# Performance work log

Measured on AMD Instinct MI355X. Metric: run time of the kernel, lower is better.

## Reference

```python
import jax, jax.numpy as jnp
import numpy as np

BLOCK_SIZE = 64
WINDOW_SIZE = 512
TOPK_BLOCKS = 16
NEG = -1e30


def setup_inputs() -> dict:
    key = jax.random.key(0)
    ks = jax.random.split(key, 6)
    B, T, D = 4, 8192, 256
    return {
        "queries": jax.random.normal(ks[0], (B, T, D), jnp.float32),
        "keys": jax.random.normal(ks[1], (B, T, D), jnp.float32),
        "values": jax.random.normal(ks[2], (B, T, D), jnp.float32),
        "gate_cmp": jax.random.uniform(ks[3], (B, T), jnp.float32),
        "gate_slc": jax.random.uniform(ks[4], (B, T), jnp.float32),
        "gate_swa": jax.random.uniform(ks[5], (B, T), jnp.float32),
    }


def _compress(x, bs):
    # mean-pool tokens into blocks of size bs (pad tail with zeros like F.pad)
    B, T, D = x.shape
    n_blocks = -(-T // bs)
    pad = n_blocks * bs - T
    if pad > 0:
        x = jnp.pad(x, ((0, 0), (0, pad), (0, 0)))
    return x.reshape(B, n_blocks, bs, D).mean(axis=2)  # [B, n_blocks, D]


def _selective(queries, comp_K, comp_V, gate):
    B, T, D = queries.shape
    nb = comp_K.shape[1]
    scale = D ** -0.5
    scores = jnp.einsum("btd,bnd->btn", queries, comp_K) * scale  # [B,T,nb]
    block_ids = jnp.arange(T) // BLOCK_SIZE                       # query's block
    allowed = jnp.arange(nb)[None, :] <= block_ids[:, None]       # no future blocks
    scores = jnp.where(allowed[None], scores, NEG)
    probs = jax.nn.softmax(scores, axis=-1)
    k = min(TOPK_BLOCKS, nb)
    topk_vals, topk_inds = jax.lax.top_k(probs, k)                # [B,T,k]
    gathered = jax.vmap(lambda cv, idx: cv[idx])(comp_V, topk_inds)  # [B,T,k,D]
    sel = jnp.einsum("btk,btkd->btd", topk_vals, gathered)
    return sel * gate[..., None]


def _sliding(queries, keys, values, gate):
    # block-banded sliding-window attention: each query attends to the last
    # WINDOW_SIZE tokens (inclusive of itself), computed per query-block of
    # size W over a 2W key window [block_start - W, block_end).
    B, T, D = queries.shape
    W = WINDOW_SIZE
    n = T // W
    scale = D ** -0.5
    k_pad = jnp.pad(keys, ((0, 0), (W, 0), (0, 0)))   # [B, T+W, D]
    v_pad = jnp.pad(values, ((0, 0), (W, 0), (0, 0)))
    idx = jnp.arange(n)[:, None] * W + jnp.arange(2 * W)[None, :]  # [n, 2W]
    k_win = k_pad[:, idx]                              # [B, n, 2W, D]
    v_win = v_pad[:, idx]
    q_blk = queries.reshape(B, n, W, D)
    scores = jnp.einsum("bnwd,bncd->bnwc", q_blk, k_win) * scale  # [B,n,W,2W]
    r = jnp.arange(W)[:, None]       # row within block
    c = jnp.arange(2 * W)[None, :]   # col within window
    base = (c <= r + W) & (c >= r + 1)                        # [W, 2W] band
    pos_ok = (jnp.arange(n)[:, None, None] * W + c[None] - W) >= 0  # [n,1,2W]
    mask = base[None] & pos_ok                                 # [n, W, 2W]
    scores = jnp.where(mask[None], scores, NEG)
    attn = jax.nn.softmax(scores, axis=-1)
    out = jnp.einsum("bnwc,bncd->bnwd", attn, v_win).reshape(B, T, D)
    return out * gate[..., None]


def reference(queries, keys, values, gate_cmp, gate_slc, gate_swa):
    D = queries.shape[-1]
    scale = D ** -0.5
    comp_K = _compress(keys, BLOCK_SIZE)
    comp_V = _compress(values, BLOCK_SIZE)
    # compressed branch (note: no causal mask, faithful to the source)
    raw = jnp.einsum("btd,bnd->btn", queries, comp_K) * scale
    comp_out = jnp.einsum("btn,bnd->btd", jax.nn.softmax(raw, axis=-1), comp_V)
    comp_out = comp_out * gate_cmp[..., None]
    sel_out = _selective(queries, comp_K, comp_V, gate_slc)
    slide_out = _sliding(queries, keys, values, gate_swa)
    return comp_out + sel_out + slide_out
```

## Files before the change

kernel.cpp:

```cpp
#include <hip/hip_runtime.h>
#include <hip/hip_bf16.h>

#define Tlen 8192
#define Dd 256
#define NBc 128

typedef __attribute__((ext_vector_type(4))) float f32x4;
typedef __attribute__((ext_vector_type(8))) short bf16x8;

__device__ __forceinline__ unsigned short f2bf(float f){
  unsigned u = __builtin_bit_cast(unsigned, f);
  u += 0x7fffu + ((u >> 16) & 1u);
  return (unsigned short)(u >> 16);
}
__device__ __forceinline__ f32x4 mfma16(bf16x8 a, bf16x8 b, f32x4 c){
  return __builtin_amdgcn_mfma_f32_16x16x32_bf16(a, b, c, 0, 0, 0);
}
__device__ __forceinline__ void bar(){
  asm volatile("" ::: "memory");
  __builtin_amdgcn_s_barrier();
  asm volatile("" ::: "memory");
}
__device__ __forceinline__ bf16x8 pack8(f32x4 a0, f32x4 a1){
  bf16x8 o;
  o[0]=(short)f2bf(a0[0]); o[1]=(short)f2bf(a0[1]); o[2]=(short)f2bf(a0[2]); o[3]=(short)f2bf(a0[3]);
  o[4]=(short)f2bf(a1[0]); o[5]=(short)f2bf(a1[1]); o[6]=(short)f2bf(a1[2]); o[7]=(short)f2bf(a1[3]);
  return o;
}
#define GLL16(g, l) __builtin_amdgcn_global_load_lds( \
    (const __attribute__((address_space(1))) unsigned int*)(const void*)(g), \
    (__attribute__((address_space(3))) unsigned int*)(void*)(l), 16, 0, 0)

template<int C>
__device__ __forceinline__ int dppi(int x){
  return __builtin_amdgcn_update_dpp(x, x, C, 0xF, 0xF, false);
}
template<int C>
__device__ __forceinline__ float dppf(float x){
  return __builtin_bit_cast(float, dppi<C>(__builtin_bit_cast(int, x)));
}
__device__ __forceinline__ float dpp_sum16(float x){
  x += dppf<0x121>(x); x += dppf<0x122>(x); x += dppf<0x124>(x); x += dppf<0x128>(x);
  return x;
}

__device__ __forceinline__ bf16x8 load_qfrag(const float* qrow, int kc, int g){
  f32x4 v0 = *(const f32x4*)(qrow + kc*32 + g*8);
  f32x4 v1 = *(const f32x4*)(qrow + kc*32 + g*8 + 4);
  return pack8(v0, v1);
}

__global__ __launch_bounds__(256) void k_prep(const float* __restrict__ K, const float* __restrict__ V,
    unsigned short* __restrict__ ck, unsigned short* __restrict__ cvt,
    unsigned short* __restrict__ Vswz, unsigned short* __restrict__ Kswz, int do_k){
  __shared__ unsigned short Lt[64][72];
  int b = blockIdx.x >> 7, blk = blockIdx.x & 127;
  int t = threadIdx.x;
  const float* Kb = K + ((size_t)b*Tlen + (size_t)blk*64)*Dd;
  const float* Vb = V + ((size_t)b*Tlen + (size_t)blk*64)*Dd;
  {
    float sk=0.f, sv=0.f;
    #pragma unroll 8
    for (int i=0;i<64;i++){ sk += Kb[(size_t)i*Dd + t]; sv += Vb[(size_t)i*Dd + t]; }
    ck[((size_t)b*NBc + blk)*Dd + (((t>>3) ^ (blk&7))<<3) + (t&7)] = f2bf(sk*(1.f/64.f));
    cvt[((size_t)b*Dd + t)*NBc + blk] = f2bf(sv*(1.f/64.f));
  }
  if (do_k){
    unsigned short* kd = Kswz + ((size_t)(b*NBc + blk))*16384;
    #pragma unroll
    for (int i=0;i<8;i++){
      int id = i*256 + t, r = id>>5, c = id&31;
      f32x4 a0 = *(const f32x4*)(Kb + (size_t)r*Dd + c*8);
      f32x4 a1 = *(const f32x4*)(Kb + (size_t)r*Dd + c*8 + 4);
      *(bf16x8*)(kd + r*256 + ((c ^ (r&7))*8)) = pack8(a0,a1);
    }
  }
  unsigned short* vd = Vswz + ((size_t)(b*NBc + blk))*16384;
  for (int dt=0; dt<4; ++dt){
    __syncthreads();
    #pragma unroll
    for (int it=0; it<4; ++it){
      int idx = it*256 + t, r = idx>>4, c4 = idx&15;
      f32x4 v = *(const f32x4*)(Vb + (size_t)r*Dd + dt*64 + c4*4);
      #pragma unroll
      for (int ii=0;ii<4;ii++) Lt[c4*4+ii][r] = f2bf(v[ii]);
    }
    __syncthreads();
    int dd = t>>2, ch = t&3, d = dt*64 + dd;
    unsigned short tmp[16];
    #pragma unroll
    for (int u=0;u<16;u++) tmp[u] = Lt[dd][ch*16+u];
    *(bf16x8*)(vd + d*64 + (((ch*2  ) ^ (d&7))*8)) = *(bf16x8*)(tmp);
    *(bf16x8*)(vd + d*64 + (((ch*2+1) ^ (d&7))*8)) = *(bf16x8*)(tmp+8);
  }
}

__device__ __forceinline__ void compsel_phase(unsigned short* LB,
    const float* Q, const unsigned short* ck, const unsigned short* cvt,
    const float* gc, const float* gs, float* out, int b, int tile, bool first){
  int q0 = tile*64;
  int t = threadIdx.x, w = t >> 6, l = t & 63, g = l >> 4, lr = l & 15;
  int tr = w >> 1, half = w & 1;

  float gcv[2], gsv[2];
  #pragma unroll
  for (int jl=0;jl<2;jl++){
    int qq = q0 + tr*16 + 4*g + half*2 + jl;
    gcv[jl] = gc[(size_t)b*Tlen + qq];
    gsv[jl] = gs[(size_t)b*Tlen + qq];
  }
  bf16x8 qa[8];
  const float* qrow = Q + ((size_t)b*Tlen + q0 + tr*16 + lr)*Dd;
  #pragma unroll
  for (int kc=0;kc<8;kc++) qa[kc] = load_qfrag(qrow, kc, g);

  __syncthreads();

  {
    const unsigned short* src = ck + (size_t)b*NBc*Dd;
    #pragma unroll
    for (int i=0;i<8;i++){
      int idx = i*512 + t;
      GLL16(src + idx*8, &LB[idx*8]);
    }
  }
  asm volatile("s_waitcnt vmcnt(0)" ::: "memory");
  bar();

  f32x4 acc[8];
  #pragma unroll
  for (int nf=0;nf<8;nf++) acc[nf] = f32x4{0.f,0.f,0.f,0.f};
  #pragma unroll
  for (int nf=0;nf<8;nf++){
    int row = nf*16+lr;
    const unsigned short* rbase = &LB[row*256];
    int xk = row & 7;
    #pragma unroll
    for (int kc=0;kc<8;kc++){
      bf16x8 bb = *(const bf16x8*)(rbase + (((kc*4+g) ^ xk)*8));
      acc[nf] = mfma16(qa[kc], bb, acc[nf]);
    }
  }
  #pragma unroll
  for (int nf=0;nf<8;nf++) acc[nf] *= 0.0625f;
  asm volatile("s_waitcnt lgkmcnt(0)" ::: "memory");
  bar();

  bool al[8];
  #pragma unroll
  for (int nf=0;nf<8;nf++) al[nf] = (nf*16+lr) <= tile;

  float e2[8][2];
  #pragma unroll
  for (int nf=0;nf<8;nf++){
    #pragma unroll
    for (int jl=0;jl<2;jl++) e2[nf][jl] = __expf(acc[nf][half*2+jl]);
  }
  float rzc[2], rzs[2];
  {
    float zc2[2]={0.f,0.f}, zs2[2]={0.f,0.f};
    #pragma unroll
    for (int nf=0;nf<8;nf++){
      #pragma unroll
      for (int jl=0;jl<2;jl++){
        zc2[jl] += e2[nf][jl];
        zs2[jl] += al[nf] ? e2[nf][jl] : 0.f;
      }
    }
    #pragma unroll
    for (int jl=0;jl<2;jl++){
      rzc[jl] = 1.f / dpp_sum16(zc2[jl]);
      rzs[jl] = 1.f / dpp_sum16(zs2[jl]);
    }
  }

  float sm2[8][2];
  #pragma unroll
  for (int nf=0;nf<8;nf++){
    #pragma unroll
    for (int jl=0;jl<2;jl++) sm2[nf][jl] = al[nf] ? acc[nf][half*2+jl] : -3e38f;
  }
  unsigned selm[2]={0,0};
  #pragma unroll 1
  for (int it=0; it<16; ++it){
    float bv[2]; int bi[2];
    #pragma unroll
    for (int jl=0;jl<2;jl++){
      float v = sm2[0][jl]; int n = lr;
      #pragma unroll
      for (int nf=1;nf<8;nf++){
        bool tk = sm2[nf][jl] > v;
        v = tk ? sm2[nf][jl] : v;
        n = tk ? nf*16+lr : n;
      }
      bv[jl]=v; bi[jl]=n;
    }
    #define DSTEP(CTRL) \
    _Pragma("unroll") \
    for (int jl=0;jl<2;jl++){ \
      float ov = dppf<CTRL>(bv[jl]); int oi = dppi<CTRL>(bi[jl]); \
      bool tk = (ov>bv[jl]) || (ov==bv[jl] && oi<bi[jl]); \
      bv[jl] = tk ? ov : bv[jl]; bi[jl] = tk ? oi : bi[jl]; \
    }
    DSTEP(0x121) DSTEP(0x122) DSTEP(0x124) DSTEP(0x128)
    #undef DSTEP
    #pragma unroll
    for (int jl=0;jl<2;jl++){
      selm[jl] |= (((bi[jl]&15)==lr) ? (1u<<(bi[jl]>>4)) : 0u);
      #pragma unroll
      for (int nf=0;nf<8;nf++)
        sm2[nf][jl] = (bi[jl] == nf*16+lr) ? -3e38f : sm2[nf][jl];
    }
  }

  unsigned short* Pc = LB;
  #pragma unroll
  for (int nf=0;nf<8;nf++){
    int n = nf*16+lr;
    #pragma unroll
    for (int jl=0;jl<2;jl++){
      float pcm = e2[nf][jl]*rzc[jl];
      float ps  = (al[nf] && ((selm[jl]>>nf)&1u)) ? e2[nf][jl]*rzs[jl] : 0.f;
      Pc[(tr*16 + 4*g + half*2 + jl)*136 + n] = f2bf(gcv[jl]*pcm + gsv[jl]*ps);
    }
  }
  __syncthreads();

  int rt = w & 3, cf = (w >> 2) * 8;
  bf16x8 pa[4];
  #pragma unroll
  for (int kc=0;kc<4;kc++) pa[kc] = *(const bf16x8*)(&Pc[(rt*16+lr)*136 + kc*32 + g*8]);
  f32x4 po[8];
  #pragma unroll
  for (int i=0;i<8;i++) po[i]=f32x4{0.f,0.f,0.f,0.f};
  const unsigned short* cvb = cvt + (size_t)b*Dd*NBc;
  #pragma unroll
  for (int i2=0;i2<8;i2++){
    int nf2 = cf + i2;
    #pragma unroll
    for (int kc=0;kc<4;kc++){
      bf16x8 vb = *(const bf16x8*)(cvb + (size_t)(nf2*16+lr)*NBc + kc*32 + g*8);
      po[i2] = mfma16(pa[kc], vb, po[i2]);
    }
  }
  #pragma unroll
  for (int i2=0;i2<8;i2++){
    #pragma unroll
    for (int j=0;j<4;j++){
      size_t o = ((size_t)b*Tlen + q0 + rt*16 + 4*g + j)*Dd + (cf+i2)*16 + lr;
      if (first) out[o] = po[i2][j];
      else       out[o] += po[i2][j];
    }
  }
}

template<bool KPRE>
__device__ __forceinline__ void swa_phase(char* RAW,
    const float* Q, const float* Kf,
    const unsigned short* Kswz, const unsigned short* Vswz,
    const float* gw, float* out, int b, int tile, bool first){
  unsigned short* K0 = (unsigned short*)RAW;
  unsigned short* Ps = (unsigned short*)(RAW + 65536);
  float* Lp = (float*)(RAW + 73728);

  int q0 = tile*64;
  int t = threadIdx.x, w = t>>6, l = t&63, g = l>>4, lr = l&15;
  int rg = w & 3, kh = w >> 2;

  bf16x8 qa[8];
  const float* qrow = Q + ((size_t)b*Tlen + q0 + rg*16 + lr)*Dd;
  #pragma unroll
  for (int kc=0;kc<8;kc++) qa[kc] = load_qfrag(qrow, kc, g);

  __syncthreads();
  asm volatile("s_waitcnt vmcnt(0)" ::: "memory");

  f32x4 po[8];
  #pragma unroll
  for (int i=0;i<8;i++) po[i]=f32x4{0.f,0.f,0.f,0.f};
  float zs[4] = {0.f,0.f,0.f,0.f};

  int jb0 = tile - 8; if (jb0 < 0) jb0 = 0;
  const int jbmax = tile;
  const size_t bof = (size_t)b*NBc*16384;

  auto stage = [&](int buf, int jb){
    const unsigned short* ks = Kswz + bof + (size_t)jb*16384 + t*8;
    #pragma unroll
    for (int i=0;i<4;i++) GLL16(ks + i*4096, &K0[buf*16384 + t*8 + i*4096]);
  };
  int cur = 0;
  if constexpr (KPRE) stage(0, jb0);

  for (int jb = jb0; jb <= jbmax; ++jb){
    if constexpr (KPRE){
      bar();
      if (jb < jbmax){
        stage(cur^1, jb+1);
        asm volatile("s_waitcnt vmcnt(4)" ::: "memory");
      } else {
        asm volatile("s_waitcnt vmcnt(0)" ::: "memory");
      }
      bar();
    } else {
      bar();
      {
        const float* kb = Kf + ((size_t)b*Tlen + (size_t)jb*64)*Dd;
        #pragma unroll
        for (int i=0;i<4;i++){
          int id = i*512 + t, r = id>>5, c = id&31;
          f32x4 a0 = *(const f32x4*)(kb + (size_t)r*Dd + c*8);
          f32x4 a1 = *(const f32x4*)(kb + (size_t)r*Dd + c*8 + 4);
          *(bf16x8*)(&K0[r*256 + ((c ^ (r&7))*8)]) = pack8(a0,a1);
        }
      }
      asm volatile("s_waitcnt vmcnt(0) lgkmcnt(0)" ::: "memory");
      bar();
    }

    f32x4 acc[2];
    acc[0]=f32x4{0.f,0.f,0.f,0.f}; acc[1]=f32x4{0.f,0.f,0.f,0.f};
    #pragma unroll
    for (int nf=0;nf<2;nf++){
      int key = kh*32 + nf*16 + lr;
      const unsigned short* rbase = &K0[cur*16384 + key*256];
      int xk = key & 7;
      #pragma unroll
      for (int kc=0;kc<8;kc++){
        bf16x8 kf = *(const bf16x8*)(rbase + (((kc*4+g) ^ xk)*8));
        acc[nf] = mfma16(qa[kc], kf, acc[nf]);
      }
    }
    #pragma unroll
    for (int nf=0;nf<2;nf++){
      int kloc = kh*32 + nf*16 + lr;
      int kglob = jb*64 + kloc;
      int kchunk = kloc >> 3;
      #pragma unroll
      for (int j=0;j<4;j++){
        int qloc = rg*16 + 4*g + j;
        int qg2 = q0 + qloc;
        float e = (kglob <= qg2 && kglob >= qg2-511) ? __expf(acc[nf][j]*0.0625f) : 0.f;
        zs[j] += e;
        Ps[qloc*64 + ((kchunk ^ (qloc&7))<<3) + (lr&7)] = f2bf(e);
      }
    }
    asm volatile("s_waitcnt lgkmcnt(0)" ::: "memory");
    bar();

    {
      bf16x8 vf[2][2];
      #pragma unroll
      for (int nf2=0;nf2<2;nf2++){
        int d = w*32 + nf2*16 + lr;
        const unsigned short* vrow = Vswz + bof + (size_t)jb*16384 + (size_t)d*64;
        int xv = d & 7;
        #pragma unroll
        for (int k2=0;k2<2;k2++)
          vf[nf2][k2] = *(const bf16x8*)(vrow + (((k2*4+g) ^ xv)*8));
      }
      #pragma unroll
      for (int rg2=0;rg2<4;rg2++){
        int qloc = rg2*16 + lr;
        int xq = qloc & 7;
        bf16x8 pa0 = *(const bf16x8*)(&Ps[qloc*64 + (((0*4+g) ^ xq)<<3)]);
        bf16x8 pa1 = *(const bf16x8*)(&Ps[qloc*64 + (((1*4+g) ^ xq)<<3)]);
        #pragma unroll
        for (int nf2=0;nf2<2;nf2++){
          po[rg2*2+nf2] = mfma16(pa0, vf[nf2][0], po[rg2*2+nf2]);
          po[rg2*2+nf2] = mfma16(pa1, vf[nf2][1], po[rg2*2+nf2]);
        }
      }
    }
    if constexpr (KPRE) cur ^= 1;
  }

  #pragma unroll
  for (int j=0;j<4;j++) zs[j] = dpp_sum16(zs[j]);
  if (lr == 0){
    #pragma unroll
    for (int j=0;j<4;j++) Lp[kh*64 + rg*16 + 4*g + j] = zs[j];
  }
  __syncthreads();

  #pragma unroll
  for (int rg2=0;rg2<4;rg2++){
    float scl[4];
    #pragma unroll
    for (int j=0;j<4;j++){
      int qloc = rg2*16 + 4*g + j;
      int q = q0 + qloc;
      scl[j] = gw[(size_t)b*Tlen + q] / (Lp[qloc] + Lp[64 + qloc]);
    }
    #pragma unroll
    for (int nf2=0;nf2<2;nf2++){
      #pragma unroll
      for (int j=0;j<4;j++){
        size_t o = ((size_t)b*Tlen + q0 + rg2*16 + 4*g + j)*Dd + w*32 + nf2*16 + lr;
        float v = po[rg2*2+nf2][j] * scl[j];
        if (first) out[o] = v;
        else       out[o] += v;
      }
    }
  }
}

template<bool KPRE>
__global__ __launch_bounds__(512,4) void k_main(const float* __restrict__ Q, const float* __restrict__ Kf,
    const unsigned short* __restrict__ ck, const unsigned short* __restrict__ cvt,
    const unsigned short* __restrict__ Kswz, const unsigned short* __restrict__ Vswz,
    const float* __restrict__ gc, const float* __restrict__ gs, const float* __restrict__ gw,
    float* __restrict__ out, int nt){
  __shared__ __align__(16) char RAW[74240];
  int wg = blockIdx.x;
  int lin = ((nt & 7) == 0) ? ((wg & 7)*(nt >> 3) + (wg >> 3)) : wg;
  int b = lin >> 7, tile = lin & 127;
  bool cfirst = (2*wg < nt);
  if (cfirst){
    compsel_phase((unsigned short*)RAW, Q, ck, cvt, gc, gs, out, b, tile, true);
    swa_phase<KPRE>(RAW, Q, Kf, Kswz, Vswz, gw, out, b, tile, false);
  } else {
    swa_phase<KPRE>(RAW, Q, Kf, Kswz, Vswz, gw, out, b, tile, true);
    compsel_phase((unsigned short*)RAW, Q, ck, cvt, gc, gs, out, b, tile, false);
  }
}

extern "C" void kernel_launch(void* const* d_in, const int* in_sizes, int n_in,
                              void* d_out, int out_size, void* d_ws, size_t ws_size,
                              hipStream_t stream) {
  const float* Q  = (const float*)d_in[0];
  const float* K  = (const float*)d_in[1];
  const float* V  = (const float*)d_in[2];
  const float* gc = (const float*)d_in[3];
  const float* gs = (const float*)d_in[4];
  const float* gwp= (const float*)d_in[5];
  float* out = (float*)d_out;
  int B = in_sizes[0] / (Tlen*Dd);

  unsigned short* ck  = (unsigned short*)d_ws;
  unsigned short* cvt = ck  + (size_t)B*NBc*Dd;
  unsigned short* Vsw = cvt + (size_t)B*Dd*NBc;
  unsigned short* Ksw = Vsw + (size_t)B*Tlen*Dd;

  size_t need_full = ((size_t)B*((size_t)NBc*Dd + (size_t)Dd*NBc + 2*(size_t)Tlen*Dd))*2;
  bool kpre = ws_size >= need_full;
  int nt = B*128;

  k_prep<<<dim3(B*128), dim3(256), 0, stream>>>(K, V, ck, cvt, Vsw, Ksw, kpre?1:0);
  if (kpre) k_main<true ><<<dim3(nt), dim3(512), 0, stream>>>(Q, K, ck, cvt, Ksw, Vsw, gc, gs, gwp, out, nt);
  else      k_main<false><<<dim3(nt), dim3(512), 0, stream>>>(Q, K, ck, cvt, Ksw, Vsw, gc, gs, gwp, out, nt);
}
```

Measured before the change: 113.7 us.

## Halve LDS tiles to double occupancy and shrink SWA key chunk to 32

The compressed-key load in the compsel phase is split into two 64-row halves, and the sliding-window loop now walks 32-key chunks instead of 64. This lets the shared-memory buffer shrink from about 74KB to 38KB, and launch bounds are raised to 8 blocks per CU to improve occupancy and latency hiding. The phase ordering is also changed to alternate by block parity. The cost is more loop iterations, more barriers and smaller MFMA batches per iteration, and the new Ps layout (stride 40, no swizzle) may cause LDS bank conflicts. The register limit from the higher occupancy target could also cause spills.

```diff
diff --git a/kernel.cpp b/kernel.cpp
--- a/kernel.cpp
+++ b/kernel.cpp
@@ -116,35 +116,36 @@
 
   __syncthreads();
 
-  {
-    const unsigned short* src = ck + (size_t)b*NBc*Dd;
-    #pragma unroll
-    for (int i=0;i<8;i++){
+  f32x4 acc[8];
+  #pragma unroll
+  for (int nf=0;nf<8;nf++) acc[nf] = f32x4{0.f,0.f,0.f,0.f};
+  #pragma unroll 1
+  for (int h=0; h<2; ++h){
+    const unsigned short* src = ck + (size_t)b*NBc*Dd + (size_t)h*64*Dd;
+    #pragma unroll
+    for (int i=0;i<4;i++){
       int idx = i*512 + t;
       GLL16(src + idx*8, &LB[idx*8]);
     }
-  }
-  asm volatile("s_waitcnt vmcnt(0)" ::: "memory");
-  bar();
-
-  f32x4 acc[8];
-  #pragma unroll
-  for (int nf=0;nf<8;nf++) acc[nf] = f32x4{0.f,0.f,0.f,0.f};
-  #pragma unroll
-  for (int nf=0;nf<8;nf++){
-    int row = nf*16+lr;
-    const unsigned short* rbase = &LB[row*256];
-    int xk = row & 7;
-    #pragma unroll
-    for (int kc=0;kc<8;kc++){
-      bf16x8 bb = *(const bf16x8*)(rbase + (((kc*4+g) ^ xk)*8));
-      acc[nf] = mfma16(qa[kc], bb, acc[nf]);
-    }
+    asm volatile("s_waitcnt vmcnt(0)" ::: "memory");
+    bar();
+    #pragma unroll
+    for (int nl=0;nl<4;nl++){
+      int nf = h*4 + nl;
+      int lrow = nl*16+lr;
+      const unsigned short* rbase = &LB[lrow*256];
+      int xk = lrow & 7;
+      #pragma unroll
+      for (int kc=0;kc<8;kc++){
+        bf16x8 bb = *(const bf16x8*)(rbase + (((kc*4+g) ^ xk)*8));
+        acc[nf] = mfma16(qa[kc], bb, acc[nf]);
+      }
+    }
+    asm volatile("s_waitcnt lgkmcnt(0)" ::: "memory");
+    bar();
   }
   #pragma unroll
   for (int nf=0;nf<8;nf++) acc[nf] *= 0.0625f;
-  asm volatile("s_waitcnt lgkmcnt(0)" ::: "memory");
-  bar();
 
   bool al[8];
   #pragma unroll
@@ -260,8 +261,8 @@
     const unsigned short* Kswz, const unsigned short* Vswz,
     const float* gw, float* out, int b, int tile, bool first){
   unsigned short* K0 = (unsigned short*)RAW;
-  unsigned short* Ps = (unsigned short*)(RAW + 65536);
-  float* Lp = (float*)(RAW + 73728);
+  unsigned short* Ps = (unsigned short*)(RAW + 32768);
+  float* Lp = (float*)(RAW + 37888);
 
   int q0 = tile*64;
   int t = threadIdx.x, w = t>>6, l = t&63, g = l>>4, lr = l&15;
@@ -280,24 +281,24 @@
   for (int i=0;i<8;i++) po[i]=f32x4{0.f,0.f,0.f,0.f};
   float zs[4] = {0.f,0.f,0.f,0.f};
 
-  int jb0 = tile - 8; if (jb0 < 0) jb0 = 0;
-  const int jbmax = tile;
+  int c0 = 2*tile - 16; if (c0 < 0) c0 = 0;
+  const int cmax = 2*tile + 1;
   const size_t bof = (size_t)b*NBc*16384;
 
-  auto stage = [&](int buf, int jb){
-    const unsigned short* ks = Kswz + bof + (size_t)jb*16384 + t*8;
-    #pragma unroll
-    for (int i=0;i<4;i++) GLL16(ks + i*4096, &K0[buf*16384 + t*8 + i*4096]);
+  auto stage = [&](int buf, int jc){
+    const unsigned short* ks = Kswz + bof + (size_t)(jc>>1)*16384 + (size_t)(jc&1)*8192 + t*8;
+    GLL16(ks, &K0[buf*8192 + t*8]);
+    GLL16(ks + 4096, &K0[buf*8192 + t*8 + 4096]);
   };
   int cur = 0;
-  if constexpr (KPRE) stage(0, jb0);
-
-  for (int jb = jb0; jb <= jbmax; ++jb){
+  if constexpr (KPRE) stage(0, c0);
+
+  for (int jc = c0; jc <= cmax; ++jc){
     if constexpr (KPRE){
       bar();
-      if (jb < jbmax){
-        stage(cur^1, jb+1);
-        asm volatile("s_waitcnt vmcnt(4)" ::: "memory");
+      if (jc < cmax){
+        stage(cur^1, jc+1);
+        asm volatile("s_waitcnt vmcnt(2)" ::: "memory");
       } else {
         asm volatile("s_waitcnt vmcnt(0)" ::: "memory");
       }
@@ -305,9 +306,9 @@
     } else {
       bar();
       {
-        const float* kb = Kf + ((size_t)b*Tlen + (size_t)jb*64)*Dd;
+        const float* kb = Kf + ((size_t)b*Tlen + (size_t)jc*32)*Dd;
         #pragma unroll
-        for (int i=0;i<4;i++){
+        for (int i=0;i<2;i++){
           int id = i*512 + t, r = id>>5, c = id&31;
           f32x4 a0 = *(const f32x4*)(kb + (size_t)r*Dd + c*8);
           f32x4 a1 = *(const f32x4*)(kb + (size_t)r*Dd + c*8 + 4);
@@ -318,58 +319,46 @@
       bar();
     }
 
-    f32x4 acc[2];
-    acc[0]=f32x4{0.f,0.f,0.f,0.f}; acc[1]=f32x4{0.f,0.f,0.f,0.f};
-    #pragma unroll
-    for (int nf=0;nf<2;nf++){
-      int key = kh*32 + nf*16 + lr;
-      const unsigned short* rbase = &K0[cur*16384 + key*256];
-      int xk = key & 7;
+    int kloc = kh*16 + lr;
+    f32x4 acc = f32x4{0.f,0.f,0.f,0.f};
+    {
+      const unsigned short* rbase = &K0[cur*8192 + kloc*256];
+      int xk = kloc & 7;
       #pragma unroll
       for (int kc=0;kc<8;kc++){
         bf16x8 kf = *(const bf16x8*)(rbase + (((kc*4+g) ^ xk)*8));
-        acc[nf] = mfma16(qa[kc], kf, acc[nf]);
-      }
-    }
-    #pragma unroll
-    for (int nf=0;nf<2;nf++){
-      int kloc = kh*32 + nf*16 + lr;
-      int kglob = jb*64 + kloc;
-      int kchunk = kloc >> 3;
+        acc = mfma16(qa[kc], kf, acc);
+      }
+    }
+    {
+      int kglob = jc*32 + kloc;
       #pragma unroll
       for (int j=0;j<4;j++){
         int qloc = rg*16 + 4*g + j;
         int qg2 = q0 + qloc;
-        float e = (kglob <= qg2 && kglob >= qg2-511) ? __expf(acc[nf][j]*0.0625f) : 0.f;
+        float e = (kglob <= qg2 && kglob >= qg2-511) ? __expf(acc[j]*0.0625f) : 0.f;
         zs[j] += e;
-        Ps[qloc*64 + ((kchunk ^ (qloc&7))<<3) + (lr&7)] = f2bf(e);
+        Ps[qloc*40 + kloc] = f2bf(e);
       }
     }
     asm volatile("s_waitcnt lgkmcnt(0)" ::: "memory");
     bar();
 
     {
-      bf16x8 vf[2][2];
+      int hc = jc & 1;
+      bf16x8 vf[2];
       #pragma unroll
       for (int nf2=0;nf2<2;nf2++){
         int d = w*32 + nf2*16 + lr;
-        const unsigned short* vrow = Vswz + bof + (size_t)jb*16384 + (size_t)d*64;
-        int xv = d & 7;
+        const unsigned short* vrow = Vswz + bof + (size_t)(jc>>1)*16384 + (size_t)d*64;
+        vf[nf2] = *(const bf16x8*)(vrow + (((hc*4+g) ^ (d&7))*8));
+      }
+      #pragma unroll
+      for (int rg2=0;rg2<4;rg2++){
+        bf16x8 pa = *(const bf16x8*)(&Ps[(rg2*16+lr)*40 + g*8]);
         #pragma unroll
-        for (int k2=0;k2<2;k2++)
-          vf[nf2][k2] = *(const bf16x8*)(vrow + (((k2*4+g) ^ xv)*8));
-      }
-      #pragma unroll
-      for (int rg2=0;rg2<4;rg2++){
-        int qloc = rg2*16 + lr;
-        int xq = qloc & 7;
-        bf16x8 pa0 = *(const bf16x8*)(&Ps[qloc*64 + (((0*4+g) ^ xq)<<3)]);
-        bf16x8 pa1 = *(const bf16x8*)(&Ps[qloc*64 + (((1*4+g) ^ xq)<<3)]);
-        #pragma unroll
-        for (int nf2=0;nf2<2;nf2++){
-          po[rg2*2+nf2] = mfma16(pa0, vf[nf2][0], po[rg2*2+nf2]);
-          po[rg2*2+nf2] = mfma16(pa1, vf[nf2][1], po[rg2*2+nf2]);
-        }
+        for (int nf2=0;nf2<2;nf2++)
+          po[rg2*2+nf2] = mfma16(pa, vf[nf2], po[rg2*2+nf2]);
       }
     }
     if constexpr (KPRE) cur ^= 1;
@@ -406,16 +395,16 @@
 }
 
 template<bool KPRE>
-__global__ __launch_bounds__(512,4) void k_main(const float* __restrict__ Q, const float* __restrict__ Kf,
+__global__ __launch_bounds__(512,8) void k_main(const float* __restrict__ Q, const float* __restrict__ Kf,
     const unsigned short* __restrict__ ck, const unsigned short* __restrict__ cvt,
     const unsigned short* __restrict__ Kswz, const unsigned short* __restrict__ Vswz,
     const float* __restrict__ gc, const float* __restrict__ gs, const float* __restrict__ gw,
     float* __restrict__ out, int nt){
-  __shared__ __align__(16) char RAW[74240];
+  __shared__ __align__(16) char RAW[38400];
   int wg = blockIdx.x;
   int lin = ((nt & 7) == 0) ? ((wg & 7)*(nt >> 3) + (wg >> 3)) : wg;
   int b = lin >> 7, tile = lin & 127;
-  bool cfirst = (2*wg < nt);
+  bool cfirst = (wg & 1);
   if (cfirst){
     compsel_phase((unsigned short*)RAW, Q, ck, cvt, gc, gs, out, b, tile, true);
     swa_phase<KPRE>(RAW, Q, Kf, Kswz, Vswz, gw, out, b, tile, false);
```

Result: slower. 306.5 us (+169.6%).

## Repartition sliding-window waves so each owns full key rows, dropping cross-wave P exchange

Applied to the files above, without the earlier changes.

Each of the 8 waves in the sliding-window phase now computes scores for a 16-query slice against all 64 keys of a block, instead of splitting keys across two wave halves. Probabilities go into a per-wave LDS slice, which removes the workgroup barrier between the QK and PV steps and the cross-wave row-sum reduction in LDS. Each wave then accumulates half of the head dimension. The costs are duplicated QK MFMA work across the two head-dim waves, larger LDS (80KB, which may lower occupancy), and V fragments read straight from global memory with more loads per wave. The compressed-first phase order also changes to alternate by workgroup parity.

```diff
diff --git a/kernel.cpp b/kernel.cpp
--- a/kernel.cpp
+++ b/kernel.cpp
@@ -261,14 +261,14 @@
     const float* gw, float* out, int b, int tile, bool first){
   unsigned short* K0 = (unsigned short*)RAW;
   unsigned short* Ps = (unsigned short*)(RAW + 65536);
-  float* Lp = (float*)(RAW + 73728);
 
   int q0 = tile*64;
   int t = threadIdx.x, w = t>>6, l = t&63, g = l>>4, lr = l&15;
-  int rg = w & 3, kh = w >> 2;
+  int qg = w >> 1, hd = w & 1;
+  unsigned short* Pw = Ps + w*1024;
 
   bf16x8 qa[8];
-  const float* qrow = Q + ((size_t)b*Tlen + q0 + rg*16 + lr)*Dd;
+  const float* qrow = Q + ((size_t)b*Tlen + q0 + qg*16 + lr)*Dd;
   #pragma unroll
   for (int kc=0;kc<8;kc++) qa[kc] = load_qfrag(qrow, kc, g);
 
@@ -318,11 +318,12 @@
       bar();
     }
 
-    f32x4 acc[2];
-    acc[0]=f32x4{0.f,0.f,0.f,0.f}; acc[1]=f32x4{0.f,0.f,0.f,0.f};
-    #pragma unroll
-    for (int nf=0;nf<2;nf++){
-      int key = kh*32 + nf*16 + lr;
+    f32x4 acc[4];
+    #pragma unroll
+    for (int nf=0;nf<4;nf++) acc[nf] = f32x4{0.f,0.f,0.f,0.f};
+    #pragma unroll
+    for (int nf=0;nf<4;nf++){
+      int key = nf*16 + lr;
       const unsigned short* rbase = &K0[cur*16384 + key*256];
       int xk = key & 7;
       #pragma unroll
@@ -332,75 +333,49 @@
       }
     }
     #pragma unroll
-    for (int nf=0;nf<2;nf++){
-      int kloc = kh*32 + nf*16 + lr;
-      int kglob = jb*64 + kloc;
-      int kchunk = kloc >> 3;
+    for (int nf=0;nf<4;nf++){
+      int key = nf*16 + lr;
+      int kglob = jb*64 + key;
+      int kch = key >> 3;
       #pragma unroll
       for (int j=0;j<4;j++){
-        int qloc = rg*16 + 4*g + j;
-        int qg2 = q0 + qloc;
-        float e = (kglob <= qg2 && kglob >= qg2-511) ? __expf(acc[nf][j]*0.0625f) : 0.f;
+        int qrw = 4*g + j;
+        int qgl = q0 + qg*16 + qrw;
+        float e = (kglob <= qgl && kglob >= qgl-511) ? __expf(acc[nf][j]*0.0625f) : 0.f;
         zs[j] += e;
-        Ps[qloc*64 + ((kchunk ^ (qloc&7))<<3) + (lr&7)] = f2bf(e);
-      }
-    }
-    asm volatile("s_waitcnt lgkmcnt(0)" ::: "memory");
-    bar();
-
-    {
-      bf16x8 vf[2][2];
-      #pragma unroll
-      for (int nf2=0;nf2<2;nf2++){
-        int d = w*32 + nf2*16 + lr;
-        const unsigned short* vrow = Vswz + bof + (size_t)jb*16384 + (size_t)d*64;
-        int xv = d & 7;
-        #pragma unroll
-        for (int k2=0;k2<2;k2++)
-          vf[nf2][k2] = *(const bf16x8*)(vrow + (((k2*4+g) ^ xv)*8));
-      }
-      #pragma unroll
-      for (int rg2=0;rg2<4;rg2++){
-        int qloc = rg2*16 + lr;
-        int xq = qloc & 7;
-        bf16x8 pa0 = *(const bf16x8*)(&Ps[qloc*64 + (((0*4+g) ^ xq)<<3)]);
-        bf16x8 pa1 = *(const bf16x8*)(&Ps[qloc*64 + (((1*4+g) ^ xq)<<3)]);
-        #pragma unroll
-        for (int nf2=0;nf2<2;nf2++){
-          po[rg2*2+nf2] = mfma16(pa0, vf[nf2][0], po[rg2*2+nf2]);
-          po[rg2*2+nf2] = mfma16(pa1, vf[nf2][1], po[rg2*2+nf2]);
-        }
-      }
+        Pw[qrw*64 + ((kch ^ (qrw&7))<<3) + (key&7)] = f2bf(e);
+      }
+    }
+    bf16x8 pa[2];
+    #pragma unroll
+    for (int kc2=0;kc2<2;kc2++)
+      pa[kc2] = *(const bf16x8*)(&Pw[lr*64 + (((kc2*4+g) ^ (lr&7))<<3)]);
+    #pragma unroll
+    for (int nf2=0;nf2<8;nf2++){
+      int d = hd*128 + nf2*16 + lr;
+      const unsigned short* vrow = Vswz + bof + (size_t)jb*16384 + (size_t)d*64;
+      int xv = d & 7;
+      bf16x8 vf0 = *(const bf16x8*)(vrow + (((0*4+g) ^ xv)*8));
+      bf16x8 vf1 = *(const bf16x8*)(vrow + (((1*4+g) ^ xv)*8));
+      po[nf2] = mfma16(pa[0], vf0, po[nf2]);
+      po[nf2] = mfma16(pa[1], vf1, po[nf2]);
     }
     if constexpr (KPRE) cur ^= 1;
   }
 
   #pragma unroll
   for (int j=0;j<4;j++) zs[j] = dpp_sum16(zs[j]);
-  if (lr == 0){
-    #pragma unroll
-    for (int j=0;j<4;j++) Lp[kh*64 + rg*16 + 4*g + j] = zs[j];
-  }
-  __syncthreads();
-
-  #pragma unroll
-  for (int rg2=0;rg2<4;rg2++){
-    float scl[4];
-    #pragma unroll
-    for (int j=0;j<4;j++){
-      int qloc = rg2*16 + 4*g + j;
-      int q = q0 + qloc;
-      scl[j] = gw[(size_t)b*Tlen + q] / (Lp[qloc] + Lp[64 + qloc]);
-    }
-    #pragma unroll
-    for (int nf2=0;nf2<2;nf2++){
-      #pragma unroll
-      for (int j=0;j<4;j++){
-        size_t o = ((size_t)b*Tlen + q0 + rg2*16 + 4*g + j)*Dd + w*32 + nf2*16 + lr;
-        float v = po[rg2*2+nf2][j] * scl[j];
-        if (first) out[o] = v;
-        else       out[o] += v;
-      }
+
+  #pragma unroll
+  for (int j=0;j<4;j++){
+    int q = q0 + qg*16 + 4*g + j;
+    float scl = gw[(size_t)b*Tlen + q] / zs[j];
+    #pragma unroll
+    for (int nf2=0;nf2<8;nf2++){
+      size_t o = ((size_t)b*Tlen + q)*Dd + hd*128 + nf2*16 + lr;
+      float v = po[nf2][j] * scl;
+      if (first) out[o] = v;
+      else       out[o] += v;
     }
   }
 }
@@ -411,11 +386,11 @@
     const unsigned short* __restrict__ Kswz, const unsigned short* __restrict__ Vswz,
     const float* __restrict__ gc, const float* __restrict__ gs, const float* __restrict__ gw,
     float* __restrict__ out, int nt){
-  __shared__ __align__(16) char RAW[74240];
+  __shared__ __align__(16) char RAW[81920];
   int wg = blockIdx.x;
   int lin = ((nt & 7) == 0) ? ((wg & 7)*(nt >> 3) + (wg >> 3)) : wg;
   int b = lin >> 7, tile = lin & 127;
-  bool cfirst = (2*wg < nt);
+  bool cfirst = (wg & 1);
   if (cfirst){
     compsel_phase((unsigned short*)RAW, Q, ck, cvt, gc, gs, out, b, tile, true);
     swa_phase<KPRE>(RAW, Q, Kf, Kswz, Vswz, gw, out, b, tile, false);
```

Result: slower. 179.3 us (+57.7%).

## Accumulate sliding-window and compressed outputs in registers, write output once

Applied to the files above, without the earlier changes.

The kernel previously ran the compressed/selective phase and the sliding-window phase in alternating order, and each phase wrote or read-modify-wrote the fp32 output in global memory. Now the sliding-window phase leaves its gated, normalized result in registers. The compressed phase is remapped so each wave covers the same output fragments (all 4 row groups times 32 columns) and accumulates into those registers before a single store. This removes one full output read and write pass, but keeps more accumulators live across phases, and the phase order is no longer alternated across workgroups. It also changes the Ps column index from lr&7 to kloc&7 and adds an unused packed-convert helper.

```diff
diff --git a/kernel.cpp b/kernel.cpp
--- a/kernel.cpp
+++ b/kernel.cpp
@@ -15,6 +15,9 @@
 }
 __device__ __forceinline__ f32x4 mfma16(bf16x8 a, bf16x8 b, f32x4 c){
   return __builtin_amdgcn_mfma_f32_16x16x32_bf16(a, b, c, 0, 0, 0);
+}
+__device__ __forceinline__ unsigned pkbf(float a, float b){
+  unsigned r; asm("v_cvt_pk_bf16_f32 %0, %1, %2" : "=v"(r) : "v"(a), "v"(b)); return r;
 }
 __device__ __forceinline__ void bar(){
   asm volatile("" ::: "memory");
@@ -95,177 +98,19 @@
   }
 }
 
-__device__ __forceinline__ void compsel_phase(unsigned short* LB,
-    const float* Q, const unsigned short* ck, const unsigned short* cvt,
-    const float* gc, const float* gs, float* out, int b, int tile, bool first){
-  int q0 = tile*64;
-  int t = threadIdx.x, w = t >> 6, l = t & 63, g = l >> 4, lr = l & 15;
-  int tr = w >> 1, half = w & 1;
-
-  float gcv[2], gsv[2];
-  #pragma unroll
-  for (int jl=0;jl<2;jl++){
-    int qq = q0 + tr*16 + 4*g + half*2 + jl;
-    gcv[jl] = gc[(size_t)b*Tlen + qq];
-    gsv[jl] = gs[(size_t)b*Tlen + qq];
-  }
-  bf16x8 qa[8];
-  const float* qrow = Q + ((size_t)b*Tlen + q0 + tr*16 + lr)*Dd;
-  #pragma unroll
-  for (int kc=0;kc<8;kc++) qa[kc] = load_qfrag(qrow, kc, g);
-
-  __syncthreads();
-
-  {
-    const unsigned short* src = ck + (size_t)b*NBc*Dd;
-    #pragma unroll
-    for (int i=0;i<8;i++){
-      int idx = i*512 + t;
-      GLL16(src + idx*8, &LB[idx*8]);
-    }
-  }
-  asm volatile("s_waitcnt vmcnt(0)" ::: "memory");
-  bar();
-
-  f32x4 acc[8];
-  #pragma unroll
-  for (int nf=0;nf<8;nf++) acc[nf] = f32x4{0.f,0.f,0.f,0.f};
-  #pragma unroll
-  for (int nf=0;nf<8;nf++){
-    int row = nf*16+lr;
-    const unsigned short* rbase = &LB[row*256];
-    int xk = row & 7;
-    #pragma unroll
-    for (int kc=0;kc<8;kc++){
-      bf16x8 bb = *(const bf16x8*)(rbase + (((kc*4+g) ^ xk)*8));
-      acc[nf] = mfma16(qa[kc], bb, acc[nf]);
-    }
-  }
-  #pragma unroll
-  for (int nf=0;nf<8;nf++) acc[nf] *= 0.0625f;
-  asm volatile("s_waitcnt lgkmcnt(0)" ::: "memory");
-  bar();
-
-  bool al[8];
-  #pragma unroll
-  for (int nf=0;nf<8;nf++) al[nf] = (nf*16+lr) <= tile;
-
-  float e2[8][2];
-  #pragma unroll
-  for (int nf=0;nf<8;nf++){
-    #pragma unroll
-    for (int jl=0;jl<2;jl++) e2[nf][jl] = __expf(acc[nf][half*2+jl]);
-  }
-  float rzc[2], rzs[2];
-  {
-    float zc2[2]={0.f,0.f}, zs2[2]={0.f,0.f};
-    #pragma unroll
-    for (int nf=0;nf<8;nf++){
-      #pragma unroll
-      for (int jl=0;jl<2;jl++){
-        zc2[jl] += e2[nf][jl];
-        zs2[jl] += al[nf] ? e2[nf][jl] : 0.f;
-      }
-    }
-    #pragma unroll
-    for (int jl=0;jl<2;jl++){
-      rzc[jl] = 1.f / dpp_sum16(zc2[jl]);
-      rzs[jl] = 1.f / dpp_sum16(zs2[jl]);
-    }
-  }
-
-  float sm2[8][2];
-  #pragma unroll
-  for (int nf=0;nf<8;nf++){
-    #pragma unroll
-    for (int jl=0;jl<2;jl++) sm2[nf][jl] = al[nf] ? acc[nf][half*2+jl] : -3e38f;
-  }
-  unsigned selm[2]={0,0};
-  #pragma unroll 1
-  for (int it=0; it<16; ++it){
-    float bv[2]; int bi[2];
-    #pragma unroll
-    for (int jl=0;jl<2;jl++){
-      float v = sm2[0][jl]; int n = lr;
-      #pragma unroll
-      for (int nf=1;nf<8;nf++){
-        bool tk = sm2[nf][jl] > v;
-        v = tk ? sm2[nf][jl] : v;
-        n = tk ? nf*16+lr : n;
-      }
-      bv[jl]=v; bi[jl]=n;
-    }
-    #define DSTEP(CTRL) \
-    _Pragma("unroll") \
-    for (int jl=0;jl<2;jl++){ \
-      float ov = dppf<CTRL>(bv[jl]); int oi = dppi<CTRL>(bi[jl]); \
-      bool tk = (ov>bv[jl]) || (ov==bv[jl] && oi<bi[jl]); \
-      bv[jl] = tk ? ov : bv[jl]; bi[jl] = tk ? oi : bi[jl]; \
-    }
-    DSTEP(0x121) DSTEP(0x122) DSTEP(0x124) DSTEP(0x128)
-    #undef DSTEP
-    #pragma unroll
-    for (int jl=0;jl<2;jl++){
-      selm[jl] |= (((bi[jl]&15)==lr) ? (1u<<(bi[jl]>>4)) : 0u);
-      #pragma unroll
-      for (int nf=0;nf<8;nf++)
-        sm2[nf][jl] = (bi[jl] == nf*16+lr) ? -3e38f : sm2[nf][jl];
-    }
-  }
-
-  unsigned short* Pc = LB;
-  #pragma unroll
-  for (int nf=0;nf<8;nf++){
-    int n = nf*16+lr;
-    #pragma unroll
-    for (int jl=0;jl<2;jl++){
-      float pcm = e2[nf][jl]*rzc[jl];
-      float ps  = (al[nf] && ((selm[jl]>>nf)&1u)) ? e2[nf][jl]*rzs[jl] : 0.f;
-      Pc[(tr*16 + 4*g + half*2 + jl)*136 + n] = f2bf(gcv[jl]*pcm + gsv[jl]*ps);
-    }
-  }
-  __syncthreads();
-
-  int rt = w & 3, cf = (w >> 2) * 8;
-  bf16x8 pa[4];
-  #pragma unroll
-  for (int kc=0;kc<4;kc++) pa[kc] = *(const bf16x8*)(&Pc[(rt*16+lr)*136 + kc*32 + g*8]);
-  f32x4 po[8];
-  #pragma unroll
-  for (int i=0;i<8;i++) po[i]=f32x4{0.f,0.f,0.f,0.f};
-  const unsigned short* cvb = cvt + (size_t)b*Dd*NBc;
-  #pragma unroll
-  for (int i2=0;i2<8;i2++){
-    int nf2 = cf + i2;
-    #pragma unroll
-    for (int kc=0;kc<4;kc++){
-      bf16x8 vb = *(const bf16x8*)(cvb + (size_t)(nf2*16+lr)*NBc + kc*32 + g*8);
-      po[i2] = mfma16(pa[kc], vb, po[i2]);
-    }
-  }
-  #pragma unroll
-  for (int i2=0;i2<8;i2++){
-    #pragma unroll
-    for (int j=0;j<4;j++){
-      size_t o = ((size_t)b*Tlen + q0 + rt*16 + 4*g + j)*Dd + (cf+i2)*16 + lr;
-      if (first) out[o] = po[i2][j];
-      else       out[o] += po[i2][j];
-    }
-  }
-}
-
 template<bool KPRE>
 __device__ __forceinline__ void swa_phase(char* RAW,
     const float* Q, const float* Kf,
     const unsigned short* Kswz, const unsigned short* Vswz,
-    const float* gw, float* out, int b, int tile, bool first){
+    const float* gw, int b, int tile, f32x4* po){
   unsigned short* K0 = (unsigned short*)RAW;
   unsigned short* Ps = (unsigned short*)(RAW + 65536);
   float* Lp = (float*)(RAW + 73728);
 
   int q0 = tile*64;
   int t = threadIdx.x, w = t>>6, l = t&63, g = l>>4, lr = l&15;
-  int rg = w & 3, kh = w >> 2;
+  int rg = w & 3;
+  int kh = w >> 2;
 
   bf16x8 qa[8];
   const float* qrow = Q + ((size_t)b*Tlen + q0 + rg*16 + lr)*Dd;
@@ -275,7 +120,6 @@
   __syncthreads();
   asm volatile("s_waitcnt vmcnt(0)" ::: "memory");
 
-  f32x4 po[8];
   #pragma unroll
   for (int i=0;i<8;i++) po[i]=f32x4{0.f,0.f,0.f,0.f};
   float zs[4] = {0.f,0.f,0.f,0.f};
@@ -342,7 +186,7 @@
         int qg2 = q0 + qloc;
         float e = (kglob <= qg2 && kglob >= qg2-511) ? __expf(acc[nf][j]*0.0625f) : 0.f;
         zs[j] += e;
-        Ps[qloc*64 + ((kchunk ^ (qloc&7))<<3) + (lr&7)] = f2bf(e);
+        Ps[qloc*64 + ((kchunk ^ (qloc&7))<<3) + (kloc&7)] = f2bf(e);
       }
     }
     asm volatile("s_waitcnt lgkmcnt(0)" ::: "memory");
@@ -382,24 +226,178 @@
     for (int j=0;j<4;j++) Lp[kh*64 + rg*16 + 4*g + j] = zs[j];
   }
   __syncthreads();
-
   #pragma unroll
   for (int rg2=0;rg2<4;rg2++){
-    float scl[4];
     #pragma unroll
     for (int j=0;j<4;j++){
       int qloc = rg2*16 + 4*g + j;
-      int q = q0 + qloc;
-      scl[j] = gw[(size_t)b*Tlen + q] / (Lp[qloc] + Lp[64 + qloc]);
-    }
+      float scl = gw[(size_t)b*Tlen + q0 + qloc] / (Lp[qloc] + Lp[64 + qloc]);
+      #pragma unroll
+      for (int nf2=0;nf2<2;nf2++) po[rg2*2+nf2][j] *= scl;
+    }
+  }
+}
+
+__device__ __forceinline__ void compsel_phase(unsigned short* LB,
+    const float* Q, const unsigned short* ck, const unsigned short* cvt,
+    const float* gc, const float* gs, float* out, int b, int tile, f32x4* po){
+  int q0 = tile*64;
+  int t = threadIdx.x, w = t >> 6, l = t & 63, g = l >> 4, lr = l & 15;
+  int tr = w >> 1, half = w & 1;
+
+  float gcv[2], gsv[2];
+  #pragma unroll
+  for (int jl=0;jl<2;jl++){
+    int qq = q0 + tr*16 + 4*g + half*2 + jl;
+    gcv[jl] = gc[(size_t)b*Tlen + qq];
+    gsv[jl] = gs[(size_t)b*Tlen + qq];
+  }
+  bf16x8 qa[8];
+  const float* qrow = Q + ((size_t)b*Tlen + q0 + tr*16 + lr)*Dd;
+  #pragma unroll
+  for (int kc=0;kc<8;kc++) qa[kc] = load_qfrag(qrow, kc, g);
+
+  __syncthreads();
+
+  {
+    const unsigned short* src = ck + (size_t)b*NBc*Dd;
+    #pragma unroll
+    for (int i=0;i<8;i++){
+      int idx = i*512 + t;
+      GLL16(src + idx*8, &LB[idx*8]);
+    }
+  }
+  asm volatile("s_waitcnt vmcnt(0)" ::: "memory");
+  bar();
+
+  f32x4 acc[8];
+  #pragma unroll
+  for (int nf=0;nf<8;nf++) acc[nf] = f32x4{0.f,0.f,0.f,0.f};
+  #pragma unroll
+  for (int nf=0;nf<8;nf++){
+    int row = nf*16+lr;
+    const unsigned short* rbase = &LB[row*256];
+    int xk = row & 7;
+    #pragma unroll
+    for (int kc=0;kc<8;kc++){
+      bf16x8 bb = *(const bf16x8*)(rbase + (((kc*4+g) ^ xk)*8));
+      acc[nf] = mfma16(qa[kc], bb, acc[nf]);
+    }
+  }
+  #pragma unroll
+  for (int nf=0;nf<8;nf++) acc[nf] *= 0.0625f;
+  asm volatile("s_waitcnt lgkmcnt(0)" ::: "memory");
+  bar();
+
+  bool al[8];
+  #pragma unroll
+  for (int nf=0;nf<8;nf++) al[nf] = (nf*16+lr) <= tile;
+
+  float e2[8][2];
+  #pragma unroll
+  for (int nf=0;nf<8;nf++){
+    #pragma unroll
+    for (int jl=0;jl<2;jl++) e2[nf][jl] = __expf(acc[nf][half*2+jl]);
+  }
+  float rzc[2], rzs[2];
+  {
+    float zc2[2]={0.f,0.f}, zs2[2]={0.f,0.f};
+    #pragma unroll
+    for (int nf=0;nf<8;nf++){
+      #pragma unroll
+      for (int jl=0;jl<2;jl++){
+        zc2[jl] += e2[nf][jl];
+        zs2[jl] += al[nf] ? e2[nf][jl] : 0.f;
+      }
+    }
+    #pragma unroll
+    for (int jl=0;jl<2;jl++){
+      rzc[jl] = 1.f / dpp_sum16(zc2[jl]);
+      rzs[jl] = 1.f / dpp_sum16(zs2[jl]);
+    }
+  }
+
+  float sm2[8][2];
+  #pragma unroll
+  for (int nf=0;nf<8;nf++){
+    #pragma unroll
+    for (int jl=0;jl<2;jl++) sm2[nf][jl] = al[nf] ? acc[nf][half*2+jl] : -3e38f;
+  }
+  unsigned selm[2]={0,0};
+  #pragma unroll 1
+  for (int it=0; it<16; ++it){
+    float bv[2]; int bi[2];
+    #pragma unroll
+    for (int jl=0;jl<2;jl++){
+      float v = sm2[0][jl]; int n = lr;
+      #pragma unroll
+      for (int nf=1;nf<8;nf++){
+        bool tk = sm2[nf][jl] > v;
+        v = tk ? sm2[nf][jl] : v;
+        n = tk ? nf*16+lr : n;
+      }
+      bv[jl]=v; bi[jl]=n;
+    }
+    #define DSTEP(CTRL) \
+    _Pragma("unroll") \
+    for (int jl=0;jl<2;jl++){ \
+      float ov = dppf<CTRL>(bv[jl]); int oi = dppi<CTRL>(bi[jl]); \
+      bool tk = (ov>bv[jl]) || (ov==bv[jl] && oi<bi[jl]); \
+      bv[jl] = tk ? ov : bv[jl]; bi[jl] = tk ? oi : bi[jl]; \
+    }
+    DSTEP(0x121) DSTEP(0x122) DSTEP(0x124) DSTEP(0x128)
+    #undef DSTEP
+    #pragma unroll
+    for (int jl=0;jl<2;jl++){
+      selm[jl] |= (((bi[jl]&15)==lr) ? (1u<<(bi[jl]>>4)) : 0u);
+      #pragma unroll
+      for (int nf=0;nf<8;nf++)
+        sm2[nf][jl] = (bi[jl] == nf*16+lr) ? -3e38f : sm2[nf][jl];
+    }
+  }
+
+  unsigned short* Pc = LB;
+  #pragma unroll
+  for (int nf=0;nf<8;nf++){
+    int n = nf*16+lr;
+    #pragma unroll
+    for (int jl=0;jl<2;jl++){
+      float pcm = e2[nf][jl]*rzc[jl];
+      float ps  = (al[nf] && ((selm[jl]>>nf)&1u)) ? e2[nf][jl]*rzs[jl] : 0.f;
+      Pc[(tr*16 + 4*g + half*2 + jl)*136 + n] = f2bf(gcv[jl]*pcm + gsv[jl]*ps);
+    }
+  }
+  __syncthreads();
+
+  const unsigned short* cvb = cvt + (size_t)b*Dd*NBc;
+  bf16x8 vb[2][4];
+  #pragma unroll
+  for (int nf2=0;nf2<2;nf2++){
+    int d = w*32 + nf2*16 + lr;
+    #pragma unroll
+    for (int kc=0;kc<4;kc++)
+      vb[nf2][kc] = *(const bf16x8*)(cvb + (size_t)d*NBc + kc*32 + g*8);
+  }
+  #pragma unroll
+  for (int rg2=0;rg2<4;rg2++){
+    bf16x8 pa[4];
+    #pragma unroll
+    for (int kc=0;kc<4;kc++)
+      pa[kc] = *(const bf16x8*)(&Pc[(rg2*16+lr)*136 + kc*32 + g*8]);
     #pragma unroll
     for (int nf2=0;nf2<2;nf2++){
       #pragma unroll
+      for (int kc=0;kc<4;kc++)
+        po[rg2*2+nf2] = mfma16(pa[kc], vb[nf2][kc], po[rg2*2+nf2]);
+    }
+  }
+  #pragma unroll
+  for (int rg2=0;rg2<4;rg2++){
+    #pragma unroll
+    for (int nf2=0;nf2<2;nf2++){
+      #pragma unroll
       for (int j=0;j<4;j++){
-        size_t o = ((size_t)b*Tlen + q0 + rg2*16 + 4*g + j)*Dd + w*32 + nf2*16 + lr;
-        float v = po[rg2*2+nf2][j] * scl[j];
-        if (first) out[o] = v;
-        else       out[o] += v;
+        out[((size_t)b*Tlen + q0 + rg2*16 + 4*g + j)*Dd + w*32 + nf2*16 + lr] = po[rg2*2+nf2][j];
       }
     }
   }
@@ -415,14 +413,9 @@
   int wg = blockIdx.x;
   int lin = ((nt & 7) == 0) ? ((wg & 7)*(nt >> 3) + (wg >> 3)) : wg;
   int b = lin >> 7, tile = lin & 127;
-  bool cfirst = (2*wg < nt);
-  if (cfirst){
-    compsel_phase((unsigned short*)RAW, Q, ck, cvt, gc, gs, out, b, tile, true);
-    swa_phase<KPRE>(RAW, Q, Kf, Kswz, Vswz, gw, out, b, tile, false);
-  } else {
-    swa_phase<KPRE>(RAW, Q, Kf, Kswz, Vswz, gw, out, b, tile, true);
-    compsel_phase((unsigned short*)RAW, Q, ck, cvt, gc, gs, out, b, tile, false);
-  }
+  f32x4 po[8];
+  swa_phase<KPRE>(RAW, Q, Kf, Kswz, Vswz, gw, b, tile, po);
+  compsel_phase((unsigned short*)RAW, Q, ck, cvt, gc, gs, out, b, tile, po);
 }
 
 extern "C" void kernel_launch(void* const* d_in, const int* in_sizes, int n_in,
```

Measured after the change: 109.5 us. 3.7% less time.
